# Optimization experiments

Hardware: AMD Instinct MI355X
Metric: run time of the kernel (lower is better)

Reference implementation:

```python
import jax, jax.numpy as jnp
import numpy as np

MARGIN = 1.0  # from init kwargs (alpha/beta unused in forward)


def setup_inputs() -> dict:
    key = jax.random.key(0)
    k1, k2 = jax.random.split(key)
    inputs = jax.random.normal(k1, (4096, 512), dtype=jnp.float32)
    targets = jax.random.randint(k2, (4096,), 0, 64)
    return {"inputs": inputs, "targets": targets}


def reference(inputs, targets):
    n = inputs.shape[0]
    mag = jnp.sum(inputs * inputs, axis=1)                      # [n]
    sim = inputs @ inputs.T                                      # [n, n]
    d2 = jax.nn.relu(mag[:, None] + mag[None, :] - 2.0 * sim)   # squared dists, clamped
    # grad-safe sqrt (diagonal is exactly 0)
    dist = jnp.where(d2 > 0, jnp.sqrt(jnp.where(d2 > 0, d2, 1.0)), 0.0)

    same = targets[:, None] == targets[None, :]
    eye = jnp.eye(n, dtype=bool)
    pos_mask = same & ~eye          # positives, diagonal removed
    neg_mask = ~same                # different labels

    # per-row sum_k exp(margin - d_ik) over negatives; the original filters
    # neg_dist.nonzero(), i.e. excludes exact-zero distances
    row_neg = jnp.sum(
        jnp.where(neg_mask & (dist != 0), jnp.exp(MARGIN - dist), 0.0), axis=1
    )                                                            # [n]

    # J_ij = log(neg_i + neg_j) + d_ij, summed over upper-triangle positive pairs
    J = jnp.log(row_neg[:, None] + row_neg[None, :]) + dist      # [n, n]
    idx = jnp.arange(n)
    triu_pos = pos_mask & (idx[:, None] < idx[None, :])
    loss = jnp.sum(jnp.where(triu_pos, jax.nn.relu(J) ** 2, 0.0))
    len_p = jnp.sum(pos_mask)  # original divides by FULL (symmetric) positive count
    return loss / len_p
```

## Files before the change

kernel.cpp:

```cpp
#include <hip/hip_runtime.h>
#include <math.h>

#define NROWS 4096
#define DIM   512
#define BM    128
#define BK    64
#define NKT   (DIM / BK)
#define NTILE (NROWS / BM)
#define NBLK  (NTILE * (NTILE + 1) / 2)

typedef __attribute__((ext_vector_type(4))) float f32x4;
typedef __attribute__((ext_vector_type(8))) short bf16x8;

#define PART_OFF 32800
#define XB_OFF   (PART_OFF + NROWS * NTILE * 2)
#define PAIR_OFF (XB_OFF + NROWS * DIM * 2)

__device__ inline unsigned short f2bf(float f) {
    unsigned int u = __float_as_uint(f);
    unsigned int r = (u + 0x7fffu + ((u >> 16) & 1u)) >> 16;
    return (unsigned short)r;
}
__device__ inline float bf2f(unsigned short u) {
    return __uint_as_float((unsigned int)u << 16);
}

__global__ void prep_kernel(const float* __restrict__ X,
                            unsigned short* __restrict__ Xb,
                            float* __restrict__ mag,
                            unsigned int* __restrict__ ctrl) {
    if (blockIdx.x == 0 && threadIdx.x < 4) ctrl[threadIdx.x] = 0u;
    int row  = blockIdx.x * 4 + (threadIdx.x >> 6);
    int lane = threadIdx.x & 63;
    const float4* p = reinterpret_cast<const float4*>(X + (size_t)row * DIM);
    short4* o = reinterpret_cast<short4*>(Xb + (size_t)row * DIM);
    float s = 0.f;
#pragma unroll
    for (int q = lane; q < DIM / 4; q += 64) {
        float4 v = p[q];
        s += v.x * v.x + v.y * v.y + v.z * v.z + v.w * v.w;
        short4 b;
        b.x = (short)f2bf(v.x); b.y = (short)f2bf(v.y);
        b.z = (short)f2bf(v.z); b.w = (short)f2bf(v.w);
        o[q] = b;
    }
#pragma unroll
    for (int off = 32; off; off >>= 1) s += __shfl_down(s, off);
    if (lane == 0) mag[row] = s;
}

__global__ __launch_bounds__(256, 3) void sim_mfma(
        const unsigned short* __restrict__ Xb, const int* __restrict__ tgt,
        const float* __restrict__ mag, unsigned short* __restrict__ part,
        unsigned int* __restrict__ pair_cnt, uint2* __restrict__ pairs,
        unsigned int cap) {
    __shared__ unsigned short As[BM * BK];
    __shared__ unsigned short Bs[BM * BK];

    const int tid  = threadIdx.x;
    const int lane = tid & 63;
    const int wid  = tid >> 6;
    const int wr   = wid >> 1, wc = wid & 1;
    const int l15  = lane & 15;
    const int lg   = lane >> 4;

    int b = blockIdx.x;
    int t = (b & 7) * 66 + (b >> 3);

    int bi = (int)((65.0f - sqrtf(4225.0f - 8.0f * (float)t)) * 0.5f);
    if (bi < 0) bi = 0;
    if (bi > NTILE - 1) bi = NTILE - 1;
    while ((65 * (bi + 1) - (bi + 1) * (bi + 1)) / 2 <= t) bi++;
    while ((65 * bi - bi * bi) / 2 > t) bi--;
    int bj = bi + (t - (65 * bi - bi * bi) / 2);
    const int rowBase = bi * BM;
    const int colBase = bj * BM;
    const bool offd = (bi != bj);

    f32x4 acc[4][4];
#pragma unroll
    for (int m = 0; m < 4; m++)
#pragma unroll
        for (int n = 0; n < 4; n++) acc[m][n] = (f32x4){0.f, 0.f, 0.f, 0.f};

#pragma unroll 1
    for (int kt = 0; kt < NKT; kt++) {
        const int k0 = kt * BK;
        __syncthreads();
#pragma unroll
        for (int c = 0; c < 4; c++) {
            int chunkBase = (c * 4 + wid) * 64;
            int idx = chunkBase + lane;
            int r   = idx >> 3;
            int ch  = idx & 7;
            int gch = ch ^ (r & 7);
            const unsigned short* ga = Xb + (size_t)(rowBase + r) * DIM + k0 + gch * 8;
            __builtin_amdgcn_global_load_lds(
                (const __attribute__((address_space(1))) void*)ga,
                (__attribute__((address_space(3))) void*)(As + chunkBase * 8),
                16, 0, 0);
            const unsigned short* gb = Xb + (size_t)(colBase + r) * DIM + k0 + gch * 8;
            __builtin_amdgcn_global_load_lds(
                (const __attribute__((address_space(1))) void*)gb,
                (__attribute__((address_space(3))) void*)(Bs + chunkBase * 8),
                16, 0, 0);
        }
        __syncthreads();

#pragma unroll
        for (int ksub = 0; ksub < 2; ksub++) {
            bf16x8 af[4], bf[4];
#pragma unroll
            for (int m = 0; m < 4; m++) {
                int ra = wr * 64 + m * 16 + l15;
                int ch = (ksub * 4 + lg) ^ (ra & 7);
                af[m] = *reinterpret_cast<const bf16x8*>(&As[ra * BK + ch * 8]);
            }
#pragma unroll
            for (int n = 0; n < 4; n++) {
                int rb = wc * 64 + n * 16 + l15;
                int ch = (ksub * 4 + lg) ^ (rb & 7);
                bf[n] = *reinterpret_cast<const bf16x8*>(&Bs[rb * BK + ch * 8]);
            }
#pragma unroll
            for (int m = 0; m < 4; m++)
#pragma unroll
                for (int n = 0; n < 4; n++)
                    acc[m][n] = __builtin_amdgcn_mfma_f32_16x16x32_bf16(
                        af[m], bf[n], acc[m][n], 0, 0, 0);
        }
    }

    int   gcol[4], tgj[4];
    float mj[4];
#pragma unroll
    for (int n = 0; n < 4; n++) {
        gcol[n] = colBase + wc * 64 + n * 16 + l15;
        tgj[n]  = tgt[gcol[n]];
        mj[n]   = mag[gcol[n]];
    }
    int   grow[4][4], tgi[4][4];
    float mi[4][4];
#pragma unroll
    for (int m = 0; m < 4; m++)
#pragma unroll
        for (int q = 0; q < 4; q++) {
            grow[m][q] = rowBase + wr * 64 + m * 16 + lg * 4 + q;
            tgi[m][q]  = tgt[grow[m][q]];
            mi[m][q]   = mag[grow[m][q]];
        }

    float negrow[4][4];
    float negcol[4] = {0.f, 0.f, 0.f, 0.f};
#pragma unroll
    for (int m = 0; m < 4; m++)
#pragma unroll
        for (int q = 0; q < 4; q++) negrow[m][q] = 0.f;

    int mycnt = 0;
#pragma unroll
    for (int m = 0; m < 4; m++)
#pragma unroll
        for (int n = 0; n < 4; n++)
#pragma unroll
            for (int q = 0; q < 4; q++) {
                float d2   = mi[m][q] + mj[n] - 2.f * acc[m][n][q];
                float dist = d2 > 0.f ? sqrtf(d2) : 0.f;
                acc[m][n][q] = dist;
                bool same = (tgi[m][q] == tgj[n]);
                if (!same) {
                    if (dist != 0.f) {
                        float e = __expf(1.0f - dist);
                        negrow[m][q] += e;
                        if (offd) negcol[n] += e;
                    }
                } else if (grow[m][q] < gcol[n]) {
                    mycnt++;
                }
            }

    __syncthreads();
    float* rowbuf = (float*)&As[0];
    float* colbuf = (float*)&As[1024];
    unsigned int* scan = (unsigned int*)&Bs[0];

#pragma unroll
    for (int m = 0; m < 4; m++)
#pragma unroll
        for (int q = 0; q < 4; q++) {
            float v = negrow[m][q];
            v += __shfl_xor(v, 1); v += __shfl_xor(v, 2);
            v += __shfl_xor(v, 4); v += __shfl_xor(v, 8);
            if (l15 == 0) rowbuf[wc * 128 + wr * 64 + m * 16 + lg * 4 + q] = v;
        }
#pragma unroll
    for (int n = 0; n < 4; n++) {
        float v = negcol[n];
        v += __shfl_xor(v, 16); v += __shfl_xor(v, 32);
        if (lg == 0) colbuf[wr * 128 + wc * 64 + n * 16 + l15] = v;
    }

    unsigned int pc = (unsigned int)mycnt;
    unsigned int incl = pc;
#pragma unroll
    for (int d = 1; d < 64; d <<= 1) {
        unsigned int tshf = __shfl_up(incl, d);
        if (lane >= d) incl += tshf;
    }
    if (lane == 63) scan[wid] = incl;
    __syncthreads();

    if (tid < BM) {
        float rv = rowbuf[tid] + rowbuf[128 + tid];
        part[(size_t)(rowBase + tid) * NTILE + bj] = f2bf(rv);
        if (offd) {
            float cv = colbuf[tid] + colbuf[128 + tid];
            part[(size_t)(colBase + tid) * NTILE + bi] = f2bf(cv);
        }
    }

    unsigned int woff = 0;
#pragma unroll
    for (int w = 0; w < 4; w++)
        if (w < wid) woff += scan[w];
    unsigned int btot = scan[0] + scan[1] + scan[2] + scan[3];
    if (tid == 0) scan[4] = btot ? atomicAdd(pair_cnt, btot) : 0u;
    __syncthreads();
    unsigned int mybase = scan[4] + woff + (incl - pc);

    if (pc) {
        unsigned int idx = mybase;
#pragma unroll
        for (int m = 0; m < 4; m++)
#pragma unroll
            for (int n = 0; n < 4; n++)
#pragma unroll
                for (int q = 0; q < 4; q++) {
                    if (tgi[m][q] == tgj[n] && grow[m][q] < gcol[n]) {
                        if (idx < cap) {
                            uint2 e;
                            e.x = ((unsigned int)grow[m][q] << 16) | (unsigned int)gcol[n];
                            e.y = (unsigned int)__float_as_int(acc[m][n][q]);
                            pairs[idx] = e;
                        }
                        idx++;
                    }
                }
    }
}

__global__ void reduce_kernel(const unsigned short* __restrict__ part,
                              float* __restrict__ row_neg) {
    int r = blockIdx.x * 256 + threadIdx.x;
    const bf16x8* p = reinterpret_cast<const bf16x8*>(part + (size_t)r * NTILE);
    float s = 0.f;
#pragma unroll
    for (int k = 0; k < 4; k++) {
        bf16x8 a = p[k];
#pragma unroll
        for (int u = 0; u < 8; u++) s += bf2f((unsigned short)a[u]);
    }
    row_neg[r] = s;
}

__global__ void pair_kernel(const uint2* __restrict__ pairs,
                            const unsigned int* __restrict__ pair_cnt,
                            const float* __restrict__ row_neg,
                            unsigned int cap, double* __restrict__ loss,
                            unsigned int* __restrict__ done,
                            float* __restrict__ out) {
    __shared__ double red[256];
    unsigned int n = *pair_cnt;
    if (n > cap) n = cap;
    double local = 0.0;
    for (unsigned int p = blockIdx.x * blockDim.x + threadIdx.x; p < n;
         p += gridDim.x * blockDim.x) {
        uint2 e = pairs[p];
        int i = (int)(e.x >> 16), j = (int)(e.x & 0xffffu);
        float d = __int_as_float((int)e.y);
        float J = logf(row_neg[i] + row_neg[j]) + d;
        if (J > 0.f) local += (double)J * (double)J;
    }
    red[threadIdx.x] = local;
    __syncthreads();
    for (int s = 128; s; s >>= 1) {
        if (threadIdx.x < (unsigned)s) red[threadIdx.x] += red[threadIdx.x + s];
        __syncthreads();
    }
    if (threadIdx.x == 0) {
        atomicAdd(loss, red[0]);
        __threadfence();
        unsigned int tk = atomicAdd(done, 1u);
        if (tk == gridDim.x - 1) {
            double l = atomicAdd(loss, 0.0);
            out[0] = (float)(l / (2.0 * (double)(*pair_cnt)));
        }
    }
}

extern "C" void kernel_launch(void* const* d_in, const int* in_sizes, int n_in,
                              void* d_out, int out_size, void* d_ws, size_t ws_size,
                              hipStream_t stream) {
    const float* X = (const float*)d_in[0];
    const int* tgt = (const int*)d_in[1];
    float* out = (float*)d_out;

    char* ws = (char*)d_ws;
    float* mag             = (float*)(ws + 0);
    float* row_neg         = (float*)(ws + 16384);
    double* loss           = (double*)(ws + 32768);
    unsigned int* pair_cnt = (unsigned int*)(ws + 32776);
    unsigned int* done     = (unsigned int*)(ws + 32780);
    unsigned int* ctrl     = (unsigned int*)(ws + 32768);
    unsigned short* part   = (unsigned short*)(ws + PART_OFF);
    unsigned short* Xb     = (unsigned short*)(ws + XB_OFF);
    uint2* pairs           = (uint2*)(ws + PAIR_OFF);
    unsigned int cap = 0;
    if (ws_size > PAIR_OFF + 8) cap = (unsigned int)((ws_size - PAIR_OFF) / 8);

    prep_kernel<<<NROWS / 4, 256, 0, stream>>>(X, Xb, mag, ctrl);

    sim_mfma<<<NBLK, 256, 0, stream>>>(Xb, tgt, mag, part, pair_cnt, pairs, cap);

    reduce_kernel<<<NROWS / 256, 256, 0, stream>>>(part, row_neg);

    pair_kernel<<<256, 256, 0, stream>>>(pairs, pair_cnt, row_neg, cap, loss,
                                         done, out);
}
```

Measured before the change: 53.74 us.

## Use full-grid 256x256 tiles with triple-buffered async LDS pipeline

Replaces the triangular grid of 128x128 tiles, which exploited symmetry, with a full 16x16 grid of 256x256 tiles. Each tile runs 512 threads and uses a three-stage global_load_lds pipeline with BK=32 and vmcnt-based waits. Column partial sums are dropped because every row now sees all columns, which simplifies the epilogue and shrinks the partial-sum buffer. In exchange the matmul and exp work roughly double, while launching exactly 256 blocks and overlapping loads with MFMA.

```diff
diff --git a/kernel.cpp b/kernel.cpp
--- a/kernel.cpp
+++ b/kernel.cpp
@@ -3,17 +3,17 @@
 
 #define NROWS 4096
 #define DIM   512
-#define BM    128
-#define BK    64
+#define BT    256
+#define BK    32
 #define NKT   (DIM / BK)
-#define NTILE (NROWS / BM)
-#define NBLK  (NTILE * (NTILE + 1) / 2)
+#define NTC   (NROWS / BT)
+#define NBLK  (NTC * NTC)
 
 typedef __attribute__((ext_vector_type(4))) float f32x4;
 typedef __attribute__((ext_vector_type(8))) short bf16x8;
 
 #define PART_OFF 32800
-#define XB_OFF   (PART_OFF + NROWS * NTILE * 2)
+#define XB_OFF   (PART_OFF + NROWS * NTC * 2)
 #define PAIR_OFF (XB_OFF + NROWS * DIM * 2)
 
 __device__ inline unsigned short f2bf(float f) {
@@ -49,155 +49,158 @@
     if (lane == 0) mag[row] = s;
 }
 
-__global__ __launch_bounds__(256, 3) void sim_mfma(
+__global__ __launch_bounds__(512, 2) void sim_mfma(
         const unsigned short* __restrict__ Xb, const int* __restrict__ tgt,
         const float* __restrict__ mag, unsigned short* __restrict__ part,
         unsigned int* __restrict__ pair_cnt, uint2* __restrict__ pairs,
         unsigned int cap) {
-    __shared__ unsigned short As[BM * BK];
-    __shared__ unsigned short Bs[BM * BK];
+    __shared__ unsigned short As[3][BT * BK];
+    __shared__ unsigned short Bs[3][BT * BK];
 
     const int tid  = threadIdx.x;
     const int lane = tid & 63;
     const int wid  = tid >> 6;
-    const int wr   = wid >> 1, wc = wid & 1;
+    const int wm   = wid >> 2;
+    const int wn   = wid & 3;
     const int l15  = lane & 15;
     const int lg   = lane >> 4;
 
-    int b = blockIdx.x;
-    int t = (b & 7) * 66 + (b >> 3);
-
-    int bi = (int)((65.0f - sqrtf(4225.0f - 8.0f * (float)t)) * 0.5f);
-    if (bi < 0) bi = 0;
-    if (bi > NTILE - 1) bi = NTILE - 1;
-    while ((65 * (bi + 1) - (bi + 1) * (bi + 1)) / 2 <= t) bi++;
-    while ((65 * bi - bi * bi) / 2 > t) bi--;
-    int bj = bi + (t - (65 * bi - bi * bi) / 2);
-    const int rowBase = bi * BM;
-    const int colBase = bj * BM;
-    const bool offd = (bi != bj);
-
-    f32x4 acc[4][4];
-#pragma unroll
-    for (int m = 0; m < 4; m++)
+    int b  = blockIdx.x;
+    int x  = b & 7, w8 = b >> 3;
+    int bi = (x >> 1) * 4 + (w8 >> 3);
+    int bj = (x & 1) * 8 + (w8 & 7);
+    const int rowBase = bi * BT;
+    const int colBase = bj * BT;
+
+    const int rL  = tid >> 2;
+    const int ch  = tid & 3;
+    const int gch = ch ^ ((rL + (rL >> 2)) & 3);
+    const unsigned short* srcA0 = Xb + (size_t)(rowBase + rL) * DIM + gch * 8;
+    const unsigned short* srcA1 = srcA0 + (size_t)128 * DIM;
+    const unsigned short* srcB0 = Xb + (size_t)(colBase + rL) * DIM + gch * 8;
+    const unsigned short* srcB1 = srcB0 + (size_t)128 * DIM;
+    const int dstOff = wid * 512;
+
+#define STAGE(bufi, kt2)                                                      \
+    {                                                                         \
+        const int k0 = (kt2) * BK;                                            \
+        __builtin_amdgcn_global_load_lds(                                     \
+            (const __attribute__((address_space(1))) void*)(srcA0 + k0),      \
+            (__attribute__((address_space(3))) void*)(&As[bufi][dstOff]),     \
+            16, 0, 0);                                                        \
+        __builtin_amdgcn_global_load_lds(                                     \
+            (const __attribute__((address_space(1))) void*)(srcA1 + k0),      \
+            (__attribute__((address_space(3))) void*)(&As[bufi][4096 + dstOff]),\
+            16, 0, 0);                                                        \
+        __builtin_amdgcn_global_load_lds(                                     \
+            (const __attribute__((address_space(1))) void*)(srcB0 + k0),      \
+            (__attribute__((address_space(3))) void*)(&Bs[bufi][dstOff]),     \
+            16, 0, 0);                                                        \
+        __builtin_amdgcn_global_load_lds(                                     \
+            (const __attribute__((address_space(1))) void*)(srcB1 + k0),      \
+            (__attribute__((address_space(3))) void*)(&Bs[bufi][4096 + dstOff]),\
+            16, 0, 0);                                                        \
+    }
+
+    f32x4 acc[8][4];
+#pragma unroll
+    for (int m = 0; m < 8; m++)
 #pragma unroll
         for (int n = 0; n < 4; n++) acc[m][n] = (f32x4){0.f, 0.f, 0.f, 0.f};
 
+    int aOff[8], bOff[4];
+#pragma unroll
+    for (int m = 0; m < 8; m++) {
+        int ra = wm * 128 + m * 16 + l15;
+        aOff[m] = ra * BK + ((lg ^ ((ra + (ra >> 2)) & 3)) * 8);
+    }
+#pragma unroll
+    for (int n = 0; n < 4; n++) {
+        int rb = wn * 64 + n * 16 + l15;
+        bOff[n] = rb * BK + ((lg ^ ((rb + (rb >> 2)) & 3)) * 8);
+    }
+
+    STAGE(0, 0)
+    STAGE(1, 1)
+
+    int buf = 0;
 #pragma unroll 1
     for (int kt = 0; kt < NKT; kt++) {
-        const int k0 = kt * BK;
-        __syncthreads();
-#pragma unroll
-        for (int c = 0; c < 4; c++) {
-            int chunkBase = (c * 4 + wid) * 64;
-            int idx = chunkBase + lane;
-            int r   = idx >> 3;
-            int ch  = idx & 7;
-            int gch = ch ^ (r & 7);
-            const unsigned short* ga = Xb + (size_t)(rowBase + r) * DIM + k0 + gch * 8;
-            __builtin_amdgcn_global_load_lds(
-                (const __attribute__((address_space(1))) void*)ga,
-                (__attribute__((address_space(3))) void*)(As + chunkBase * 8),
-                16, 0, 0);
-            const unsigned short* gb = Xb + (size_t)(colBase + r) * DIM + k0 + gch * 8;
-            __builtin_amdgcn_global_load_lds(
-                (const __attribute__((address_space(1))) void*)gb,
-                (__attribute__((address_space(3))) void*)(Bs + chunkBase * 8),
-                16, 0, 0);
-        }
-        __syncthreads();
-
-#pragma unroll
-        for (int ksub = 0; ksub < 2; ksub++) {
-            bf16x8 af[4], bf[4];
-#pragma unroll
-            for (int m = 0; m < 4; m++) {
-                int ra = wr * 64 + m * 16 + l15;
-                int ch = (ksub * 4 + lg) ^ (ra & 7);
-                af[m] = *reinterpret_cast<const bf16x8*>(&As[ra * BK + ch * 8]);
-            }
-#pragma unroll
-            for (int n = 0; n < 4; n++) {
-                int rb = wc * 64 + n * 16 + l15;
-                int ch = (ksub * 4 + lg) ^ (rb & 7);
-                bf[n] = *reinterpret_cast<const bf16x8*>(&Bs[rb * BK + ch * 8]);
-            }
-#pragma unroll
-            for (int m = 0; m < 4; m++)
-#pragma unroll
-                for (int n = 0; n < 4; n++)
-                    acc[m][n] = __builtin_amdgcn_mfma_f32_16x16x32_bf16(
-                        af[m], bf[n], acc[m][n], 0, 0, 0);
-        }
-    }
+        if (kt < NKT - 1) asm volatile("s_waitcnt vmcnt(4)" ::: "memory");
+        else              asm volatile("s_waitcnt vmcnt(0)" ::: "memory");
+        __builtin_amdgcn_s_barrier();
+        __builtin_amdgcn_sched_barrier(0);
+
+        if (kt + 2 < NKT) {
+            int bufS = (buf >= 1) ? buf - 1 : 2;
+            STAGE(bufS, kt + 2)
+        }
+
+        const unsigned short* Ab = &As[buf][0];
+        const unsigned short* Bb = &Bs[buf][0];
+        bf16x8 bf[4], af[8];
+#pragma unroll
+        for (int n = 0; n < 4; n++)
+            bf[n] = *reinterpret_cast<const bf16x8*>(Bb + bOff[n]);
+#pragma unroll
+        for (int m = 0; m < 8; m++)
+            af[m] = *reinterpret_cast<const bf16x8*>(Ab + aOff[m]);
+#pragma unroll
+        for (int m = 0; m < 8; m++)
+#pragma unroll
+            for (int n = 0; n < 4; n++)
+                acc[m][n] = __builtin_amdgcn_mfma_f32_16x16x32_bf16(
+                    af[m], bf[n], acc[m][n], 0, 0, 0);
+
+        buf = (buf == 2) ? 0 : buf + 1;
+    }
+#undef STAGE
+
+    __syncthreads();
+    float* rowpart = (float*)&As[0][0];
+    unsigned int* scan = (unsigned int*)&Bs[0][0];
 
     int   gcol[4], tgj[4];
     float mj[4];
 #pragma unroll
     for (int n = 0; n < 4; n++) {
-        gcol[n] = colBase + wc * 64 + n * 16 + l15;
+        gcol[n] = colBase + wn * 64 + n * 16 + l15;
         tgj[n]  = tgt[gcol[n]];
         mj[n]   = mag[gcol[n]];
     }
-    int   grow[4][4], tgi[4][4];
-    float mi[4][4];
-#pragma unroll
-    for (int m = 0; m < 4; m++)
+
+    int mycnt = 0;
+#pragma unroll
+    for (int m = 0; m < 8; m++) {
+        int   grow_[4], tgi_[4];
+        float mi_[4];
 #pragma unroll
         for (int q = 0; q < 4; q++) {
-            grow[m][q] = rowBase + wr * 64 + m * 16 + lg * 4 + q;
-            tgi[m][q]  = tgt[grow[m][q]];
-            mi[m][q]   = mag[grow[m][q]];
-        }
-
-    float negrow[4][4];
-    float negcol[4] = {0.f, 0.f, 0.f, 0.f};
-#pragma unroll
-    for (int m = 0; m < 4; m++)
-#pragma unroll
-        for (int q = 0; q < 4; q++) negrow[m][q] = 0.f;
-
-    int mycnt = 0;
-#pragma unroll
-    for (int m = 0; m < 4; m++)
+            grow_[q] = rowBase + wm * 128 + m * 16 + lg * 4 + q;
+            tgi_[q]  = tgt[grow_[q]];
+            mi_[q]   = mag[grow_[q]];
+        }
+        float negq[4] = {0.f, 0.f, 0.f, 0.f};
 #pragma unroll
         for (int n = 0; n < 4; n++)
 #pragma unroll
             for (int q = 0; q < 4; q++) {
-                float d2   = mi[m][q] + mj[n] - 2.f * acc[m][n][q];
+                float d2   = mi_[q] + mj[n] - 2.f * acc[m][n][q];
                 float dist = d2 > 0.f ? sqrtf(d2) : 0.f;
                 acc[m][n][q] = dist;
-                bool same = (tgi[m][q] == tgj[n]);
-                if (!same) {
-                    if (dist != 0.f) {
-                        float e = __expf(1.0f - dist);
-                        negrow[m][q] += e;
-                        if (offd) negcol[n] += e;
-                    }
-                } else if (grow[m][q] < gcol[n]) {
+                if (tgi_[q] != tgj[n]) {
+                    if (dist != 0.f) negq[q] += __expf(1.0f - dist);
+                } else if (grow_[q] < gcol[n]) {
                     mycnt++;
                 }
             }
-
-    __syncthreads();
-    float* rowbuf = (float*)&As[0];
-    float* colbuf = (float*)&As[1024];
-    unsigned int* scan = (unsigned int*)&Bs[0];
-
-#pragma unroll
-    for (int m = 0; m < 4; m++)
 #pragma unroll
         for (int q = 0; q < 4; q++) {
-            float v = negrow[m][q];
+            float v = negq[q];
             v += __shfl_xor(v, 1); v += __shfl_xor(v, 2);
             v += __shfl_xor(v, 4); v += __shfl_xor(v, 8);
-            if (l15 == 0) rowbuf[wc * 128 + wr * 64 + m * 16 + lg * 4 + q] = v;
-        }
-#pragma unroll
-    for (int n = 0; n < 4; n++) {
-        float v = negcol[n];
-        v += __shfl_xor(v, 16); v += __shfl_xor(v, 32);
-        if (lg == 0) colbuf[wr * 128 + wc * 64 + n * 16 + l15] = v;
+            if (l15 == 0) rowpart[wn * 256 + wm * 128 + m * 16 + lg * 4 + q] = v;
+        }
     }
 
     unsigned int pc = (unsigned int)mycnt;
@@ -210,52 +213,58 @@
     if (lane == 63) scan[wid] = incl;
     __syncthreads();
 
-    if (tid < BM) {
-        float rv = rowbuf[tid] + rowbuf[128 + tid];
-        part[(size_t)(rowBase + tid) * NTILE + bj] = f2bf(rv);
-        if (offd) {
-            float cv = colbuf[tid] + colbuf[128 + tid];
-            part[(size_t)(colBase + tid) * NTILE + bi] = f2bf(cv);
-        }
+    if (tid < BT) {
+        float s = rowpart[tid] + rowpart[256 + tid] + rowpart[512 + tid] +
+                  rowpart[768 + tid];
+        part[(size_t)(rowBase + tid) * NTC + bj] = f2bf(s);
     }
 
     unsigned int woff = 0;
 #pragma unroll
-    for (int w = 0; w < 4; w++)
+    for (int w = 0; w < 8; w++)
         if (w < wid) woff += scan[w];
-    unsigned int btot = scan[0] + scan[1] + scan[2] + scan[3];
-    if (tid == 0) scan[4] = btot ? atomicAdd(pair_cnt, btot) : 0u;
+    unsigned int btot = 0;
+#pragma unroll
+    for (int w = 0; w < 8; w++) btot += scan[w];
+    if (tid == 0) scan[8] = btot ? atomicAdd(pair_cnt, btot) : 0u;
     __syncthreads();
-    unsigned int mybase = scan[4] + woff + (incl - pc);
+    unsigned int mybase = scan[8] + woff + (incl - pc);
 
     if (pc) {
         unsigned int idx = mybase;
 #pragma unroll
-        for (int m = 0; m < 4; m++)
+        for (int m = 0; m < 8; m++) {
+            int grow_[4], tgi_[4];
+#pragma unroll
+            for (int q = 0; q < 4; q++) {
+                grow_[q] = rowBase + wm * 128 + m * 16 + lg * 4 + q;
+                tgi_[q]  = tgt[grow_[q]];
+            }
 #pragma unroll
             for (int n = 0; n < 4; n++)
 #pragma unroll
                 for (int q = 0; q < 4; q++) {
-                    if (tgi[m][q] == tgj[n] && grow[m][q] < gcol[n]) {
+                    if (tgi_[q] == tgj[n] && grow_[q] < gcol[n]) {
                         if (idx < cap) {
                             uint2 e;
-                            e.x = ((unsigned int)grow[m][q] << 16) | (unsigned int)gcol[n];
+                            e.x = ((unsigned int)grow_[q] << 16) | (unsigned int)gcol[n];
                             e.y = (unsigned int)__float_as_int(acc[m][n][q]);
                             pairs[idx] = e;
                         }
                         idx++;
                     }
                 }
+        }
     }
 }
 
 __global__ void reduce_kernel(const unsigned short* __restrict__ part,
                               float* __restrict__ row_neg) {
     int r = blockIdx.x * 256 + threadIdx.x;
-    const bf16x8* p = reinterpret_cast<const bf16x8*>(part + (size_t)r * NTILE);
+    const bf16x8* p = reinterpret_cast<const bf16x8*>(part + (size_t)r * NTC);
     float s = 0.f;
 #pragma unroll
-    for (int k = 0; k < 4; k++) {
+    for (int k = 0; k < 2; k++) {
         bf16x8 a = p[k];
 #pragma unroll
         for (int u = 0; u < 8; u++) s += bf2f((unsigned short)a[u]);
@@ -320,7 +329,7 @@
 
     prep_kernel<<<NROWS / 4, 256, 0, stream>>>(X, Xb, mag, ctrl);
 
-    sim_mfma<<<NBLK, 256, 0, stream>>>(Xb, tgt, mag, part, pair_cnt, pairs, cap);
+    sim_mfma<<<NBLK, 512, 0, stream>>>(Xb, tgt, mag, part, pair_cnt, pairs, cap);
 
     reduce_kernel<<<NROWS / 256, 256, 0, stream>>>(part, row_neg);
 
```

Measured after the change: 85.66 us. 1.59x slower.

## Switch Gram matrix from bf16 to int8 MFMA with global absmax quantization

Applied to the files above, without the earlier changes.

Quantizes the inputs to int8 with a single global scale found by a new absmax pass, and computes the similarity tile with i32 16x16x64 int8 MFMA instead of bf16. Squared norms are computed exactly in integers from the quantized values. The goal is to halve operand bytes and double MFMA throughput per instruction. It adds an extra full read of X plus a memset, and the coarse 8-bit quantization with one global scale may noticeably change distances and the loss.

```diff
diff --git a/kernel.cpp b/kernel.cpp
--- a/kernel.cpp
+++ b/kernel.cpp
@@ -4,17 +4,21 @@
 #define NROWS 4096
 #define DIM   512
 #define BM    128
-#define BK    64
-#define NKT   (DIM / BK)
+#define BKB   128
+#define NKT   (DIM / BKB)
 #define NTILE (NROWS / BM)
 #define NBLK  (NTILE * (NTILE + 1) / 2)
 
 typedef __attribute__((ext_vector_type(4))) float f32x4;
+typedef __attribute__((ext_vector_type(4))) int   i32x4;
 typedef __attribute__((ext_vector_type(8))) short bf16x8;
 
-#define PART_OFF 32800
-#define XB_OFF   (PART_OFF + NROWS * NTILE * 2)
-#define PAIR_OFF (XB_OFF + NROWS * DIM * 2)
+#define CTRL_OFF 0
+#define MAGI_OFF 64
+#define RN_OFF   (MAGI_OFF + NROWS * 4)
+#define PART_OFF (RN_OFF + NROWS * 4)
+#define XQ_OFF   (PART_OFF + NROWS * NTILE * 2)
+#define PAIR_OFF (XQ_OFF + NROWS * DIM)
 
 __device__ inline unsigned short f2bf(float f) {
     unsigned int u = __float_as_uint(f);
@@ -25,37 +29,56 @@
     return __uint_as_float((unsigned int)u << 16);
 }
 
-__global__ void prep_kernel(const float* __restrict__ X,
-                            unsigned short* __restrict__ Xb,
-                            float* __restrict__ mag,
-                            unsigned int* __restrict__ ctrl) {
-    if (blockIdx.x == 0 && threadIdx.x < 4) ctrl[threadIdx.x] = 0u;
+__global__ void absmax_kernel(const float* __restrict__ X,
+                              unsigned int* __restrict__ absmax_u) {
+    float m = 0.f;
+    for (int i = blockIdx.x * blockDim.x + threadIdx.x; i < NROWS * DIM / 4;
+         i += gridDim.x * blockDim.x) {
+        float4 v = reinterpret_cast<const float4*>(X)[i];
+        m = fmaxf(m, fmaxf(fmaxf(fabsf(v.x), fabsf(v.y)),
+                           fmaxf(fabsf(v.z), fabsf(v.w))));
+    }
+#pragma unroll
+    for (int o = 32; o; o >>= 1) m = fmaxf(m, __shfl_down(m, o));
+    if ((threadIdx.x & 63) == 0)
+        atomicMax(absmax_u, __float_as_uint(m));
+}
+
+__global__ void quant_kernel(const float* __restrict__ X,
+                             signed char* __restrict__ Xq,
+                             int* __restrict__ mag,
+                             const unsigned int* __restrict__ absmax_u) {
+    float absm = __uint_as_float(*absmax_u);
+    float s = absm > 1e-20f ? 126.0f / absm : 1.0f;
     int row  = blockIdx.x * 4 + (threadIdx.x >> 6);
     int lane = threadIdx.x & 63;
     const float4* p = reinterpret_cast<const float4*>(X + (size_t)row * DIM);
-    short4* o = reinterpret_cast<short4*>(Xb + (size_t)row * DIM);
-    float s = 0.f;
+    unsigned int* o = reinterpret_cast<unsigned int*>(Xq + (size_t)row * DIM);
+    int acc = 0;
 #pragma unroll
     for (int q = lane; q < DIM / 4; q += 64) {
         float4 v = p[q];
-        s += v.x * v.x + v.y * v.y + v.z * v.z + v.w * v.w;
-        short4 b;
-        b.x = (short)f2bf(v.x); b.y = (short)f2bf(v.y);
-        b.z = (short)f2bf(v.z); b.w = (short)f2bf(v.w);
-        o[q] = b;
-    }
-#pragma unroll
-    for (int off = 32; off; off >>= 1) s += __shfl_down(s, off);
-    if (lane == 0) mag[row] = s;
+        int c0 = (int)rintf(v.x * s), c1 = (int)rintf(v.y * s);
+        int c2 = (int)rintf(v.z * s), c3 = (int)rintf(v.w * s);
+        c0 = max(-127, min(127, c0)); c1 = max(-127, min(127, c1));
+        c2 = max(-127, min(127, c2)); c3 = max(-127, min(127, c3));
+        acc += c0 * c0 + c1 * c1 + c2 * c2 + c3 * c3;
+        o[q] = (unsigned int)(c0 & 255) | ((unsigned int)(c1 & 255) << 8) |
+               ((unsigned int)(c2 & 255) << 16) | ((unsigned int)(c3 & 255) << 24);
+    }
+#pragma unroll
+    for (int off = 32; off; off >>= 1) acc += __shfl_down(acc, off);
+    if (lane == 0) mag[row] = acc;
 }
 
 __global__ __launch_bounds__(256, 3) void sim_mfma(
-        const unsigned short* __restrict__ Xb, const int* __restrict__ tgt,
-        const float* __restrict__ mag, unsigned short* __restrict__ part,
+        const signed char* __restrict__ Xq, const int* __restrict__ tgt,
+        const int* __restrict__ mag, const unsigned int* __restrict__ absmax_u,
+        unsigned short* __restrict__ part,
         unsigned int* __restrict__ pair_cnt, uint2* __restrict__ pairs,
         unsigned int cap) {
-    __shared__ unsigned short As[BM * BK];
-    __shared__ unsigned short Bs[BM * BK];
+    __shared__ signed char As[BM * BKB];
+    __shared__ signed char Bs[BM * BKB];
 
     const int tid  = threadIdx.x;
     const int lane = tid & 63;
@@ -64,9 +87,10 @@
     const int l15  = lane & 15;
     const int lg   = lane >> 4;
 
+    const float inv_s = __uint_as_float(*absmax_u) * (1.0f / 126.0f);
+
     int b = blockIdx.x;
     int t = (b & 7) * 66 + (b >> 3);
-
     int bi = (int)((65.0f - sqrtf(4225.0f - 8.0f * (float)t)) * 0.5f);
     if (bi < 0) bi = 0;
     if (bi > NTILE - 1) bi = NTILE - 1;
@@ -77,15 +101,15 @@
     const int colBase = bj * BM;
     const bool offd = (bi != bj);
 
-    f32x4 acc[4][4];
-#pragma unroll
-    for (int m = 0; m < 4; m++)
-#pragma unroll
-        for (int n = 0; n < 4; n++) acc[m][n] = (f32x4){0.f, 0.f, 0.f, 0.f};
+    i32x4 acc[4][4];
+#pragma unroll
+    for (int m = 0; m < 4; m++)
+#pragma unroll
+        for (int n = 0; n < 4; n++) acc[m][n] = (i32x4){0, 0, 0, 0};
 
 #pragma unroll 1
     for (int kt = 0; kt < NKT; kt++) {
-        const int k0 = kt * BK;
+        const int k0 = kt * BKB;
         __syncthreads();
 #pragma unroll
         for (int c = 0; c < 4; c++) {
@@ -94,53 +118,51 @@
             int r   = idx >> 3;
             int ch  = idx & 7;
             int gch = ch ^ (r & 7);
-            const unsigned short* ga = Xb + (size_t)(rowBase + r) * DIM + k0 + gch * 8;
+            const signed char* ga = Xq + (size_t)(rowBase + r) * DIM + k0 + gch * 16;
             __builtin_amdgcn_global_load_lds(
                 (const __attribute__((address_space(1))) void*)ga,
-                (__attribute__((address_space(3))) void*)(As + chunkBase * 8),
+                (__attribute__((address_space(3))) void*)(As + chunkBase * 16),
                 16, 0, 0);
-            const unsigned short* gb = Xb + (size_t)(colBase + r) * DIM + k0 + gch * 8;
+            const signed char* gb = Xq + (size_t)(colBase + r) * DIM + k0 + gch * 16;
             __builtin_amdgcn_global_load_lds(
                 (const __attribute__((address_space(1))) void*)gb,
-                (__attribute__((address_space(3))) void*)(Bs + chunkBase * 8),
+                (__attribute__((address_space(3))) void*)(Bs + chunkBase * 16),
                 16, 0, 0);
         }
         __syncthreads();
 
 #pragma unroll
         for (int ksub = 0; ksub < 2; ksub++) {
-            bf16x8 af[4], bf[4];
+            i32x4 af[4], bf[4];
 #pragma unroll
             for (int m = 0; m < 4; m++) {
                 int ra = wr * 64 + m * 16 + l15;
-                int ch = (ksub * 4 + lg) ^ (ra & 7);
-                af[m] = *reinterpret_cast<const bf16x8*>(&As[ra * BK + ch * 8]);
+                int cs = (ksub * 4 + lg) ^ (ra & 7);
+                af[m] = *reinterpret_cast<const i32x4*>(&As[ra * BKB + cs * 16]);
             }
 #pragma unroll
             for (int n = 0; n < 4; n++) {
                 int rb = wc * 64 + n * 16 + l15;
-                int ch = (ksub * 4 + lg) ^ (rb & 7);
-                bf[n] = *reinterpret_cast<const bf16x8*>(&Bs[rb * BK + ch * 8]);
+                int cs = (ksub * 4 + lg) ^ (rb & 7);
+                bf[n] = *reinterpret_cast<const i32x4*>(&Bs[rb * BKB + cs * 16]);
             }
 #pragma unroll
             for (int m = 0; m < 4; m++)
 #pragma unroll
                 for (int n = 0; n < 4; n++)
-                    acc[m][n] = __builtin_amdgcn_mfma_f32_16x16x32_bf16(
+                    acc[m][n] = __builtin_amdgcn_mfma_i32_16x16x64_i8(
                         af[m], bf[n], acc[m][n], 0, 0, 0);
         }
     }
 
-    int   gcol[4], tgj[4];
-    float mj[4];
+    int gcol[4], tgj[4], mj[4];
 #pragma unroll
     for (int n = 0; n < 4; n++) {
         gcol[n] = colBase + wc * 64 + n * 16 + l15;
         tgj[n]  = tgt[gcol[n]];
         mj[n]   = mag[gcol[n]];
     }
-    int   grow[4][4], tgi[4][4];
-    float mi[4][4];
+    int grow[4][4], tgi[4][4], mi[4][4];
 #pragma unroll
     for (int m = 0; m < 4; m++)
 #pragma unroll
@@ -164,12 +186,11 @@
         for (int n = 0; n < 4; n++)
 #pragma unroll
             for (int q = 0; q < 4; q++) {
-                float d2   = mi[m][q] + mj[n] - 2.f * acc[m][n][q];
-                float dist = d2 > 0.f ? sqrtf(d2) : 0.f;
-                acc[m][n][q] = dist;
-                bool same = (tgi[m][q] == tgj[n]);
-                if (!same) {
-                    if (dist != 0.f) {
+                int   d2   = mi[m][q] + mj[n] - 2 * acc[m][n][q];
+                float dist = d2 > 0 ? sqrtf((float)d2) * inv_s : 0.f;
+                acc[m][n][q] = __float_as_int(dist);
+                if (tgi[m][q] != tgj[n]) {
+                    if (d2 > 0) {
                         float e = __expf(1.0f - dist);
                         negrow[m][q] += e;
                         if (offd) negcol[n] += e;
@@ -181,7 +202,7 @@
 
     __syncthreads();
     float* rowbuf = (float*)&As[0];
-    float* colbuf = (float*)&As[1024];
+    float* colbuf = (float*)&As[1024 * 2];
     unsigned int* scan = (unsigned int*)&Bs[0];
 
 #pragma unroll
@@ -240,7 +261,7 @@
                         if (idx < cap) {
                             uint2 e;
                             e.x = ((unsigned int)grow[m][q] << 16) | (unsigned int)gcol[n];
-                            e.y = (unsigned int)__float_as_int(acc[m][n][q]);
+                            e.y = (unsigned int)acc[m][n][q];
                             pairs[idx] = e;
                         }
                         idx++;
@@ -306,21 +327,26 @@
     float* out = (float*)d_out;
 
     char* ws = (char*)d_ws;
-    float* mag             = (float*)(ws + 0);
-    float* row_neg         = (float*)(ws + 16384);
-    double* loss           = (double*)(ws + 32768);
-    unsigned int* pair_cnt = (unsigned int*)(ws + 32776);
-    unsigned int* done     = (unsigned int*)(ws + 32780);
-    unsigned int* ctrl     = (unsigned int*)(ws + 32768);
-    unsigned short* part   = (unsigned short*)(ws + PART_OFF);
-    unsigned short* Xb     = (unsigned short*)(ws + XB_OFF);
-    uint2* pairs           = (uint2*)(ws + PAIR_OFF);
+    double* loss            = (double*)(ws + CTRL_OFF);
+    unsigned int* pair_cnt  = (unsigned int*)(ws + CTRL_OFF + 8);
+    unsigned int* done      = (unsigned int*)(ws + CTRL_OFF + 12);
+    unsigned int* absmax_u  = (unsigned int*)(ws + CTRL_OFF + 16);
+    int* mag                = (int*)(ws + MAGI_OFF);
+    float* row_neg          = (float*)(ws + RN_OFF);
+    unsigned short* part    = (unsigned short*)(ws + PART_OFF);
+    signed char* Xq         = (signed char*)(ws + XQ_OFF);
+    uint2* pairs            = (uint2*)(ws + PAIR_OFF);
     unsigned int cap = 0;
     if (ws_size > PAIR_OFF + 8) cap = (unsigned int)((ws_size - PAIR_OFF) / 8);
 
-    prep_kernel<<<NROWS / 4, 256, 0, stream>>>(X, Xb, mag, ctrl);
-
-    sim_mfma<<<NBLK, 256, 0, stream>>>(Xb, tgt, mag, part, pair_cnt, pairs, cap);
+    hipMemsetAsync(ws + CTRL_OFF, 0, 32, stream);
+
+    absmax_kernel<<<256, 256, 0, stream>>>(X, absmax_u);
+
+    quant_kernel<<<NROWS / 4, 256, 0, stream>>>(X, Xq, mag, absmax_u);
+
+    sim_mfma<<<NBLK, 256, 0, stream>>>(Xq, tgt, mag, absmax_u, part, pair_cnt,
+                                       pairs, cap);
 
     reduce_kernel<<<NROWS / 256, 256, 0, stream>>>(part, row_neg);
 
```

New measurement: 68.21 us. +26.9%, slower.
